# Kernel tuning notes

Measured on AMD Instinct MI355X. Metric: run time of the kernel, lower is better.

## Reference

```python
import jax, jax.numpy as jnp
import numpy as np

N_NODES = 150000   # n_users + n_entities
N_EDGES = 4800000  # nnz of sparse A_in (avg degree 32)
EMBED_DIM = 64
CONV_DIMS = [64, 32, 16]  # [embed_dim] + conv_dim_list
EPS = 1e-12  # F.normalize eps


def setup_inputs() -> dict:
    key = jax.random.key(0)
    ks = jax.random.split(key, 12)
    inp = {
        "E": jax.random.normal(ks[0], (N_NODES, EMBED_DIM), jnp.float32) * 0.1,
        "edge_vals": jax.random.uniform(ks[1], (N_EDGES,), jnp.float32),
        "rows": jax.random.randint(ks[2], (N_EDGES,), 0, N_NODES),
        "cols": jax.random.randint(ks[3], (N_EDGES,), 0, N_NODES),
    }
    i = 4
    for l in range(len(CONV_DIMS) - 1):
        din, dout = CONV_DIMS[l], CONV_DIMS[l + 1]
        scale = 1.0 / np.sqrt(din)
        inp[f"W1_{l}"] = jax.random.normal(ks[i], (dout, din), jnp.float32) * scale
        inp[f"b1_{l}"] = jax.random.normal(ks[i + 1], (dout,), jnp.float32) * 0.01
        inp[f"W2_{l}"] = jax.random.normal(ks[i + 2], (dout, din), jnp.float32) * scale
        inp[f"b2_{l}"] = jax.random.normal(ks[i + 3], (dout,), jnp.float32) * 0.01
        i += 4
    return inp


def _cf_embeddings(E, edge_vals, rows, cols, layer_params):
    """UIR_KG.calc_cf_embeddings: sparse A_in @ x, then KGAT bi-interaction."""
    N = E.shape[0]
    x = E
    outs = [x]
    for (W1, b1, W2, b2) in layer_params:
        # side = A_in @ x  as gather -> weight -> scatter-add over COO edges
        msgs = edge_vals[:, None] * x[cols]              # [n_edges, d]
        side = jax.ops.segment_sum(msgs, rows, num_segments=N)  # [N, d]
        sum_emb = jax.nn.leaky_relu((x + side) @ W1.T + b1)     # Linear1 + LeakyReLU
        bi_emb = jax.nn.leaky_relu((x * side) @ W2.T + b2)      # Linear2 + LeakyReLU
        x = sum_emb + bi_emb
        norm = jnp.linalg.norm(x, axis=1, keepdims=True)        # F.normalize(p=2, dim=1)
        outs.append(x / jnp.maximum(norm, EPS))
    return jnp.concatenate(outs, axis=1)  # [N, 64+32+16]


def reference(E, edge_vals, W1_0, b1_0, W2_0, b2_0, W1_1, b1_1, W2_1, b2_1, rows, cols):
    params = [(W1_0, b1_0, W2_0, b2_0), (W1_1, b1_1, W2_1, b2_1)]
    return _cf_embeddings(E, edge_vals, rows, cols, params)
```

## Files before the change

### kernel.cpp

```cpp
#include <hip/hip_runtime.h>


constexpr int PSHIFT = 9;
constexpr int PROWS  = 1 << PSHIFT;
constexpr int PBINS  = 512;
constexpr int GF_T   = 1024;
constexpr int GF_E   = 4096;
constexpr int GF_K   = GF_E / GF_T;

static __device__ __forceinline__ float leaky(float v) {
    return v > 0.0f ? v : 0.01f * v;
}

static __device__ __forceinline__ unsigned short f2bf_rne(float f) {
    unsigned u = __float_as_uint(f);
    return (unsigned short)((u + 0x7FFF + ((u >> 16) & 1)) >> 16);
}

static __device__ __forceinline__ float bf2f(unsigned short s) {
    return __uint_as_float(((unsigned)s) << 16);
}

__global__ void copy_E_kernel(const float* __restrict__ E, float* __restrict__ out,
                              unsigned short* __restrict__ Ebf, int N) {
    int tid = blockIdx.x * blockDim.x + threadIdx.x;
    if (tid >= N * 16) return;
    int i = tid >> 4, g = tid & 15;
    float4 v = reinterpret_cast<const float4*>(E)[(size_t)i * 16 + g];
    *reinterpret_cast<float4*>(out + (size_t)i * 112 + g * 4) = v;
    if (Ebf) {
        ushort4 b;
        b.x = f2bf_rne(v.x); b.y = f2bf_rne(v.y);
        b.z = f2bf_rne(v.z); b.w = f2bf_rne(v.w);
        *reinterpret_cast<ushort4*>(Ebf + (size_t)i * 64 + g * 4) = b;
    }
}

__global__ void part_hist_kernel(const int* __restrict__ rows, int* __restrict__ pcnt,
                                 int NE, int P) {
    extern __shared__ int h[];
    for (int i = threadIdx.x; i < P; i += blockDim.x) h[i] = 0;
    __syncthreads();
    for (int e = blockIdx.x * blockDim.x + threadIdx.x; e < NE; e += gridDim.x * blockDim.x)
        atomicAdd(&h[rows[e] >> PSHIFT], 1);
    __syncthreads();
    for (int i = threadIdx.x; i < P; i += blockDim.x) {
        int c = h[i];
        if (c) atomicAdd(&pcnt[i], c);
    }
}

__global__ __launch_bounds__(PBINS) void part_scan_kernel(
    const int* __restrict__ pcnt, int* __restrict__ pbase,
    int* __restrict__ gcur, int P, int NE) {
    __shared__ int s[PBINS];
    int v = (threadIdx.x < (unsigned)P) ? pcnt[threadIdx.x] : 0;
    s[threadIdx.x] = v;
    __syncthreads();
    for (int off = 1; off < PBINS; off <<= 1) {
        int t = (threadIdx.x >= (unsigned)off) ? s[threadIdx.x - off] : 0;
        __syncthreads();
        s[threadIdx.x] += t;
        __syncthreads();
    }
    if (threadIdx.x < (unsigned)P) {
        int ex = s[threadIdx.x] - v;
        pbase[threadIdx.x] = ex;
        gcur[threadIdx.x]  = ex;
    }
    if (threadIdx.x == 0) pbase[P] = NE;
}

__global__ __launch_bounds__(GF_T) void group_flush_kernel(
    const int* __restrict__ rows, const int* __restrict__ cols,
    const float* __restrict__ ev, int* __restrict__ gcur,
    int2* __restrict__ tmp, int NE, int P) {
    __shared__ int2 staged[GF_E];
    __shared__ unsigned short sp[GF_E];
    __shared__ int hist[PBINS], runstart[PBINS], hcur[PBINS], gbase[PBINS], scanb[PBINS];

    int e0  = blockIdx.x * GF_E;
    int cnt = min(GF_E, NE - e0);

    if (threadIdx.x < PBINS) hist[threadIdx.x] = 0;
    __syncthreads();

    int pk[GF_K], ck[GF_K], rk[GF_K];
    float vk[GF_K];
#pragma unroll
    for (int k = 0; k < GF_K; k++) {
        int idx = threadIdx.x + k * GF_T;
        if (idx < cnt) {
            int r = rows[e0 + idx];
            pk[k] = r >> PSHIFT;
            rk[k] = r & (PROWS - 1);
            ck[k] = cols[e0 + idx];
            vk[k] = ev[e0 + idx];
            atomicAdd(&hist[pk[k]], 1);
        } else pk[k] = -1;
    }
    __syncthreads();
    if (threadIdx.x < PBINS) scanb[threadIdx.x] = hist[threadIdx.x];
    __syncthreads();
    for (int off = 1; off < PBINS; off <<= 1) {
        int t = 0;
        if (threadIdx.x < PBINS && threadIdx.x >= (unsigned)off) t = scanb[threadIdx.x - off];
        __syncthreads();
        if (threadIdx.x < PBINS) scanb[threadIdx.x] += t;
        __syncthreads();
    }
    if (threadIdx.x < PBINS) {
        int ex = scanb[threadIdx.x] - hist[threadIdx.x];
        runstart[threadIdx.x] = ex;
        hcur[threadIdx.x]     = ex;
    }
    __syncthreads();
#pragma unroll
    for (int k = 0; k < GF_K; k++) {
        if (pk[k] >= 0) {
            int slot = atomicAdd(&hcur[pk[k]], 1);
            staged[slot] = make_int2(ck[k] | (rk[k] << 18), __float_as_int(vk[k]));
            sp[slot] = (unsigned short)pk[k];
        }
    }
    __syncthreads();
    if (threadIdx.x < (unsigned)P) {
        int h = hist[threadIdx.x];
        if (h > 0) gbase[threadIdx.x] = atomicAdd(&gcur[threadIdx.x], h);
    }
    __syncthreads();
#pragma unroll
    for (int k = 0; k < GF_K; k++) {
        int i = threadIdx.x + k * GF_T;
        if (i < cnt) {
            int p = sp[i];
            tmp[gbase[p] + (i - runstart[p])] = staged[i];
        }
    }
}

__global__ __launch_bounds__(PROWS) void row_sort_kernel(
    const int2* __restrict__ tmp, int2* __restrict__ pairs,
    const int* __restrict__ pbase, int* __restrict__ row_end, int N) {
    __shared__ int hist[PROWS], cur[PROWS], scanb[PROWS];
    int p     = blockIdx.x;
    int start = pbase[p];
    int end   = pbase[p + 1];
    hist[threadIdx.x] = 0;
    __syncthreads();
    for (int e = start + threadIdx.x; e < end; e += PROWS)
        atomicAdd(&hist[tmp[e].x >> 18], 1);
    __syncthreads();
    scanb[threadIdx.x] = hist[threadIdx.x];
    __syncthreads();
    for (int off = 1; off < PROWS; off <<= 1) {
        int t = (threadIdx.x >= (unsigned)off) ? scanb[threadIdx.x - off] : 0;
        __syncthreads();
        scanb[threadIdx.x] += t;
        __syncthreads();
    }
    int inc = scanb[threadIdx.x];
    cur[threadIdx.x] = start + inc - hist[threadIdx.x];
    int row = (p << PSHIFT) + threadIdx.x;
    if (row < N) row_end[row] = start + inc;
    __syncthreads();
    for (int e = start + threadIdx.x; e < end; e += PROWS) {
        int2 t = tmp[e];
        int pos = atomicAdd(&cur[t.x >> 18], 1);
        pairs[pos] = make_int2(t.x & 0x3FFFF, t.y);
    }
}

template<int DIN, int DOUT>
__global__ __launch_bounds__(256) void pull_layer_bf16_kernel(
    const float* __restrict__ x, const unsigned short* __restrict__ xb,
    const int2* __restrict__ pairs, const int* __restrict__ row_end,
    const float* __restrict__ W1, const float* __restrict__ b1,
    const float* __restrict__ W2, const float* __restrict__ b2,
    float* __restrict__ xnext, unsigned short* __restrict__ xnextb,
    float* __restrict__ out, int out_col0, int N) {
    constexpr int Q   = DIN / 4;
    constexpr int RPB = 256 / Q;
    constexpr int LD  = DIN + 4;
    constexpr int LD4 = LD / 4;
    static_assert(DOUT == 2 * Q, "thread owns exactly 2 output dims");

    __shared__ float sW1[DOUT * LD];
    __shared__ float sW2[DOUT * LD];
    __shared__ float hb[2][RPB][LD];

    for (int idx = threadIdx.x; idx < DOUT * DIN; idx += 256) {
        int j = idx / DIN, k = idx % DIN;
        sW1[j * LD + k] = W1[idx];
        sW2[j * LD + k] = W2[idx];
    }

    int lr  = threadIdx.x / Q;
    int q   = threadIdx.x % Q;
    int row = blockIdx.x * RPB + lr;

    if (row < N) {
        int start = row ? row_end[row - 1] : 0;
        int end   = row_end[row];
        const ushort4* xbv = reinterpret_cast<const ushort4*>(xb);
        float4 acc = make_float4(0.f, 0.f, 0.f, 0.f);
        int e = start;
        for (; e + 7 < end; e += 8) {
            int2 p[8]; ushort4 g[8];
#pragma unroll
            for (int k = 0; k < 8; k++) p[k] = pairs[e + k];
#pragma unroll
            for (int k = 0; k < 8; k++) g[k] = xbv[(size_t)p[k].x * Q + q];
#pragma unroll
            for (int k = 0; k < 8; k++) {
                float v = __int_as_float(p[k].y);
                acc.x += v * bf2f(g[k].x); acc.y += v * bf2f(g[k].y);
                acc.z += v * bf2f(g[k].z); acc.w += v * bf2f(g[k].w);
            }
        }
        for (; e < end; e++) {
            int2 p0 = pairs[e];
            ushort4 g0 = xbv[(size_t)p0.x * Q + q];
            float v0 = __int_as_float(p0.y);
            acc.x += v0 * bf2f(g0.x); acc.y += v0 * bf2f(g0.y);
            acc.z += v0 * bf2f(g0.z); acc.w += v0 * bf2f(g0.w);
        }
        const float4* xv = reinterpret_cast<const float4*>(x);
        float4 xr = xv[(size_t)row * Q + q];
        float4 h1 = make_float4(xr.x + acc.x, xr.y + acc.y, xr.z + acc.z, xr.w + acc.w);
        float4 h2 = make_float4(xr.x * acc.x, xr.y * acc.y, xr.z * acc.z, xr.w * acc.w);
        *reinterpret_cast<float4*>(&hb[0][lr][q * 4]) = h1;
        *reinterpret_cast<float4*>(&hb[1][lr][q * 4]) = h2;
    }
    __syncthreads();
    if (row >= N) return;

    float a0 = b1[q], a1 = b1[q + Q], a2 = b2[q], a3 = b2[q + Q];
    const float4* w1v = reinterpret_cast<const float4*>(sW1);
    const float4* w2v = reinterpret_cast<const float4*>(sW2);
    const float4* h1v = reinterpret_cast<const float4*>(&hb[0][lr][0]);
    const float4* h2v = reinterpret_cast<const float4*>(&hb[1][lr][0]);
#pragma unroll
    for (int k4 = 0; k4 < DIN / 4; k4++) {
        float4 h1 = h1v[k4];
        float4 h2 = h2v[k4];
        float4 wa = w1v[q * LD4 + k4];
        float4 wb = w1v[(q + Q) * LD4 + k4];
        float4 wc = w2v[q * LD4 + k4];
        float4 wd = w2v[(q + Q) * LD4 + k4];
        a0 += h1.x * wa.x + h1.y * wa.y + h1.z * wa.z + h1.w * wa.w;
        a1 += h1.x * wb.x + h1.y * wb.y + h1.z * wb.z + h1.w * wb.w;
        a2 += h2.x * wc.x + h2.y * wc.y + h2.z * wc.z + h2.w * wc.w;
        a3 += h2.x * wd.x + h2.y * wd.y + h2.z * wd.z + h2.w * wd.w;
    }
    float y0 = leaky(a0) + leaky(a2);
    float y1 = leaky(a1) + leaky(a3);
    float nrm = y0 * y0 + y1 * y1;
#pragma unroll
    for (int m = 1; m < Q; m <<= 1) nrm += __shfl_xor(nrm, m, 64);
    float inv = 1.0f / fmaxf(sqrtf(nrm), 1e-12f);
    if (xnext) {
        xnext[(size_t)row * DOUT + q]     = y0;
        xnext[(size_t)row * DOUT + q + Q] = y1;
    }
    if (xnextb) {
        xnextb[(size_t)row * DOUT + q]     = f2bf_rne(y0);
        xnextb[(size_t)row * DOUT + q + Q] = f2bf_rne(y1);
    }
    float* o = out + (size_t)row * 112 + out_col0;
    o[q]     = y0 * inv;
    o[q + Q] = y1 * inv;
}

template<int DIN, int DOUT>
__global__ __launch_bounds__(256) void pull_layer_kernel(
    const float* __restrict__ x, const int2* __restrict__ pairs,
    const int* __restrict__ row_end,
    const float* __restrict__ W1, const float* __restrict__ b1,
    const float* __restrict__ W2, const float* __restrict__ b2,
    float* __restrict__ xnext, float* __restrict__ out, int out_col0, int N) {
    constexpr int Q   = DIN / 4;
    constexpr int RPB = 256 / Q;
    constexpr int LD  = DIN + 4;
    constexpr int LD4 = LD / 4;
    static_assert(DOUT == 2 * Q, "thread owns exactly 2 output dims");

    __shared__ float sW1[DOUT * LD];
    __shared__ float sW2[DOUT * LD];
    __shared__ float hb[2][RPB][LD];

    for (int idx = threadIdx.x; idx < DOUT * DIN; idx += 256) {
        int j = idx / DIN, k = idx % DIN;
        sW1[j * LD + k] = W1[idx];
        sW2[j * LD + k] = W2[idx];
    }

    int lr  = threadIdx.x / Q;
    int q   = threadIdx.x % Q;
    int row = blockIdx.x * RPB + lr;

    if (row < N) {
        int start = row ? row_end[row - 1] : 0;
        int end   = row_end[row];
        const float4* xv = reinterpret_cast<const float4*>(x);
        float4 acc = make_float4(0.f, 0.f, 0.f, 0.f);
        int e = start;
        for (; e + 3 < end; e += 4) {
            int2 p0 = pairs[e];
            int2 p1 = pairs[e + 1];
            int2 p2 = pairs[e + 2];
            int2 p3 = pairs[e + 3];
            float4 g0 = xv[(size_t)p0.x * Q + q];
            float4 g1 = xv[(size_t)p1.x * Q + q];
            float4 g2 = xv[(size_t)p2.x * Q + q];
            float4 g3 = xv[(size_t)p3.x * Q + q];
            float v0 = __int_as_float(p0.y), v1 = __int_as_float(p1.y);
            float v2 = __int_as_float(p2.y), v3 = __int_as_float(p3.y);
            acc.x += v0 * g0.x; acc.y += v0 * g0.y; acc.z += v0 * g0.z; acc.w += v0 * g0.w;
            acc.x += v1 * g1.x; acc.y += v1 * g1.y; acc.z += v1 * g1.z; acc.w += v1 * g1.w;
            acc.x += v2 * g2.x; acc.y += v2 * g2.y; acc.z += v2 * g2.z; acc.w += v2 * g2.w;
            acc.x += v3 * g3.x; acc.y += v3 * g3.y; acc.z += v3 * g3.z; acc.w += v3 * g3.w;
        }
        for (; e < end; e++) {
            int2 p0 = pairs[e];
            float4 g0 = xv[(size_t)p0.x * Q + q];
            float v0 = __int_as_float(p0.y);
            acc.x += v0 * g0.x; acc.y += v0 * g0.y; acc.z += v0 * g0.z; acc.w += v0 * g0.w;
        }
        float4 xr = xv[(size_t)row * Q + q];
        float4 h1 = make_float4(xr.x + acc.x, xr.y + acc.y, xr.z + acc.z, xr.w + acc.w);
        float4 h2 = make_float4(xr.x * acc.x, xr.y * acc.y, xr.z * acc.z, xr.w * acc.w);
        *reinterpret_cast<float4*>(&hb[0][lr][q * 4]) = h1;
        *reinterpret_cast<float4*>(&hb[1][lr][q * 4]) = h2;
    }
    __syncthreads();
    if (row >= N) return;

    float a0 = b1[q], a1 = b1[q + Q], a2 = b2[q], a3 = b2[q + Q];
    const float4* w1v = reinterpret_cast<const float4*>(sW1);
    const float4* w2v = reinterpret_cast<const float4*>(sW2);
    const float4* h1v = reinterpret_cast<const float4*>(&hb[0][lr][0]);
    const float4* h2v = reinterpret_cast<const float4*>(&hb[1][lr][0]);
#pragma unroll
    for (int k4 = 0; k4 < DIN / 4; k4++) {
        float4 h1 = h1v[k4];
        float4 h2 = h2v[k4];
        float4 wa = w1v[q * LD4 + k4];
        float4 wb = w1v[(q + Q) * LD4 + k4];
        float4 wc = w2v[q * LD4 + k4];
        float4 wd = w2v[(q + Q) * LD4 + k4];
        a0 += h1.x * wa.x + h1.y * wa.y + h1.z * wa.z + h1.w * wa.w;
        a1 += h1.x * wb.x + h1.y * wb.y + h1.z * wb.z + h1.w * wb.w;
        a2 += h2.x * wc.x + h2.y * wc.y + h2.z * wc.z + h2.w * wc.w;
        a3 += h2.x * wd.x + h2.y * wd.y + h2.z * wd.z + h2.w * wd.w;
    }
    float y0 = leaky(a0) + leaky(a2);
    float y1 = leaky(a1) + leaky(a3);
    float nrm = y0 * y0 + y1 * y1;
#pragma unroll
    for (int m = 1; m < Q; m <<= 1) nrm += __shfl_xor(nrm, m, 64);
    float inv = 1.0f / fmaxf(sqrtf(nrm), 1e-12f);
    if (xnext) {
        xnext[(size_t)row * DOUT + q]     = y0;
        xnext[(size_t)row * DOUT + q + Q] = y1;
    }
    float* o = out + (size_t)row * 112 + out_col0;
    o[q]     = y0 * inv;
    o[q + Q] = y1 * inv;
}

extern "C" void kernel_launch(void* const* d_in, const int* in_sizes, int n_in,
                              void* d_out, int out_size, void* d_ws, size_t ws_size,
                              hipStream_t stream) {
    const float* Eemb = (const float*)d_in[0];
    const float* ev   = (const float*)d_in[1];
    const int*   rows = (const int*)d_in[2];
    const int*   cols = (const int*)d_in[3];
    const float* W1_0 = (const float*)d_in[4];
    const float* b1_0 = (const float*)d_in[5];
    const float* W2_0 = (const float*)d_in[6];
    const float* b2_0 = (const float*)d_in[7];
    const float* W1_1 = (const float*)d_in[8];
    const float* b1_1 = (const float*)d_in[9];
    const float* W2_1 = (const float*)d_in[10];
    const float* b2_1 = (const float*)d_in[11];
    float* out = (float*)d_out;

    int N  = in_sizes[0] / 64;
    int NE = in_sizes[1];
    int P  = (N + PROWS - 1) >> PSHIFT;

    size_t pairs_b  = (size_t)NE * sizeof(int2);
    size_t rowend_b = ((size_t)N * sizeof(int) + 255) & ~(size_t)255;
    size_t small_b  = (PBINS + (PBINS + 1) + PBINS) * sizeof(int) + 256;
    small_b = (small_b + 255) & ~(size_t)255;
    size_t x1_b     = ((size_t)N * 32 * sizeof(float) + 255) & ~(size_t)255;
    size_t ebf_b    = ((size_t)N * 64 * sizeof(unsigned short) + 255) & ~(size_t)255;
    size_t x1b_b    = (size_t)N * 32 * sizeof(unsigned short);

    char* base = (char*)d_ws;
    int2*  pairs   = (int2*)base;
    int*   row_end = (int*)(base + pairs_b);
    int*   pcnt    = (int*)(base + pairs_b + rowend_b);
    int*   pbase   = pcnt + PBINS;
    int*   gcur    = pbase + PBINS + 1;
    float* x1      = (float*)(base + pairs_b + rowend_b + small_b);
    unsigned short* Ebf = (unsigned short*)(base + pairs_b + rowend_b + small_b + x1_b);
    unsigned short* x1b = (unsigned short*)(base + pairs_b + rowend_b + small_b + x1_b + ebf_b);

    bool use_bf  = ws_size >= pairs_b + rowend_b + small_b + x1_b + ebf_b;
    bool use_bf1 = use_bf && ws_size >= pairs_b + rowend_b + small_b + x1_b + ebf_b + x1b_b;

    int2* tmp = (int2*)d_out;

    hipMemsetAsync(pcnt, 0, PBINS * sizeof(int), stream);
    part_hist_kernel<<<256, 1024, P * sizeof(int), stream>>>(rows, pcnt, NE, P);
    part_scan_kernel<<<1, PBINS, 0, stream>>>(pcnt, pbase, gcur, P, NE);
    group_flush_kernel<<<(NE + GF_E - 1) / GF_E, GF_T, 0, stream>>>(
        rows, cols, ev, gcur, tmp, NE, P);
    row_sort_kernel<<<P, PROWS, 0, stream>>>(tmp, pairs, pbase, row_end, N);

    copy_E_kernel<<<(N * 16 + 255) / 256, 256, 0, stream>>>(
        Eemb, out, use_bf ? Ebf : nullptr, N);

    if (use_bf) {
        pull_layer_bf16_kernel<64, 32><<<(N + 15) / 16, 256, 0, stream>>>(
            Eemb, Ebf, pairs, row_end, W1_0, b1_0, W2_0, b2_0,
            x1, use_bf1 ? x1b : nullptr, out, 64, N);
    } else {
        pull_layer_kernel<64, 32><<<(N + 15) / 16, 256, 0, stream>>>(
            Eemb, pairs, row_end, W1_0, b1_0, W2_0, b2_0, x1, out, 64, N);
    }
    if (use_bf1) {
        pull_layer_bf16_kernel<32, 16><<<(N + 31) / 32, 256, 0, stream>>>(
            x1, x1b, pairs, row_end, W1_1, b1_1, W2_1, b2_1,
            nullptr, nullptr, out, 96, N);
    } else {
        pull_layer_kernel<32, 16><<<(N + 31) / 32, 256, 0, stream>>>(
            x1, pairs, row_end, W1_1, b1_1, W2_1, b2_1, nullptr, out, 96, N);
    }
}
```

Measured before the change: 350.6 us.

## Widen bf16 gathers to 8 elements per thread and drop fp32 self-row reads

The pull-layer kernel now has each thread gather 8 bf16 features per edge with a 16-byte load instead of 4 with an 8-byte load. This halves the threads per row, doubles the rows per block, and issues fewer, wider gather transactions. The self row is read from the bf16 copy instead of the fp32 embedding, and the intermediate sums are staged in shared memory as bf16. Each thread now computes 4 contiguous outputs, so the output and next-layer writes are vectorized. The layer-1 fp32 buffer is no longer written, which cuts memory traffic, but bf16 rounding of x and of the hidden sums adds error.

After: 356.8 us. Within noise of the previous version (+1.8%).

```diff
diff --git a/kernel.cpp b/kernel.cpp
--- a/kernel.cpp
+++ b/kernel.cpp
@@ -17,8 +17,13 @@
     return (unsigned short)((u + 0x7FFF + ((u >> 16) & 1)) >> 16);
 }
 
-static __device__ __forceinline__ float bf2f(unsigned short s) {
-    return __uint_as_float(((unsigned)s) << 16);
+static __device__ __forceinline__ void unpack2(unsigned u, float& lo, float& hi) {
+    lo = __uint_as_float(u << 16);
+    hi = __uint_as_float(u & 0xFFFF0000u);
+}
+
+static __device__ __forceinline__ unsigned pack2(float lo, float hi) {
+    return ((unsigned)f2bf_rne(hi) << 16) | (unsigned)f2bf_rne(lo);
 }
 
 __global__ void copy_E_kernel(const float* __restrict__ E, float* __restrict__ out,
@@ -172,27 +177,28 @@
 }
 
 template<int DIN, int DOUT>
-__global__ __launch_bounds__(256) void pull_layer_bf16_kernel(
-    const float* __restrict__ x, const unsigned short* __restrict__ xb,
+__global__ __launch_bounds__(256) void pull_layer_b2_kernel(
+    const unsigned short* __restrict__ xb,
     const int2* __restrict__ pairs, const int* __restrict__ row_end,
     const float* __restrict__ W1, const float* __restrict__ b1,
     const float* __restrict__ W2, const float* __restrict__ b2,
-    float* __restrict__ xnext, unsigned short* __restrict__ xnextb,
+    unsigned short* __restrict__ xnextb,
     float* __restrict__ out, int out_col0, int N) {
-    constexpr int Q   = DIN / 4;
+    constexpr int Q   = DIN / 8;
     constexpr int RPB = 256 / Q;
-    constexpr int LD  = DIN + 4;
-    constexpr int LD4 = LD / 4;
-    static_assert(DOUT == 2 * Q, "thread owns exactly 2 output dims");
-
-    __shared__ float sW1[DOUT * LD];
-    __shared__ float sW2[DOUT * LD];
-    __shared__ float hb[2][RPB][LD];
+    constexpr int JT  = DOUT / Q;
+    constexpr int LDU = DIN + 8;
+    constexpr int LDW = DIN + 4;
+    static_assert(JT == 4, "thread owns 4 contiguous outputs");
+
+    __shared__ float sW1[DOUT * LDW];
+    __shared__ float sW2[DOUT * LDW];
+    __shared__ unsigned short hb[2][RPB][LDU];
 
     for (int idx = threadIdx.x; idx < DOUT * DIN; idx += 256) {
         int j = idx / DIN, k = idx % DIN;
-        sW1[j * LD + k] = W1[idx];
-        sW2[j * LD + k] = W2[idx];
+        sW1[j * LDW + k] = W1[idx];
+        sW2[j * LDW + k] = W2[idx];
     }
 
     int lr  = threadIdx.x / Q;
@@ -202,11 +208,11 @@
     if (row < N) {
         int start = row ? row_end[row - 1] : 0;
         int end   = row_end[row];
-        const ushort4* xbv = reinterpret_cast<const ushort4*>(xb);
-        float4 acc = make_float4(0.f, 0.f, 0.f, 0.f);
+        const uint4* xbv = reinterpret_cast<const uint4*>(xb);
+        float acc[8] = {0.f, 0.f, 0.f, 0.f, 0.f, 0.f, 0.f, 0.f};
         int e = start;
         for (; e + 7 < end; e += 8) {
-            int2 p[8]; ushort4 g[8];
+            int2 p[8]; uint4 g[8];
 #pragma unroll
             for (int k = 0; k < 8; k++) p[k] = pairs[e + k];
 #pragma unroll
@@ -214,62 +220,86 @@
 #pragma unroll
             for (int k = 0; k < 8; k++) {
                 float v = __int_as_float(p[k].y);
-                acc.x += v * bf2f(g[k].x); acc.y += v * bf2f(g[k].y);
-                acc.z += v * bf2f(g[k].z); acc.w += v * bf2f(g[k].w);
+                float lo, hi;
+                unpack2(g[k].x, lo, hi); acc[0] += v * lo; acc[1] += v * hi;
+                unpack2(g[k].y, lo, hi); acc[2] += v * lo; acc[3] += v * hi;
+                unpack2(g[k].z, lo, hi); acc[4] += v * lo; acc[5] += v * hi;
+                unpack2(g[k].w, lo, hi); acc[6] += v * lo; acc[7] += v * hi;
             }
         }
         for (; e < end; e++) {
             int2 p0 = pairs[e];
-            ushort4 g0 = xbv[(size_t)p0.x * Q + q];
+            uint4 g0 = xbv[(size_t)p0.x * Q + q];
             float v0 = __int_as_float(p0.y);
-            acc.x += v0 * bf2f(g0.x); acc.y += v0 * bf2f(g0.y);
-            acc.z += v0 * bf2f(g0.z); acc.w += v0 * bf2f(g0.w);
-        }
-        const float4* xv = reinterpret_cast<const float4*>(x);
-        float4 xr = xv[(size_t)row * Q + q];
-        float4 h1 = make_float4(xr.x + acc.x, xr.y + acc.y, xr.z + acc.z, xr.w + acc.w);
-        float4 h2 = make_float4(xr.x * acc.x, xr.y * acc.y, xr.z * acc.z, xr.w * acc.w);
-        *reinterpret_cast<float4*>(&hb[0][lr][q * 4]) = h1;
-        *reinterpret_cast<float4*>(&hb[1][lr][q * 4]) = h2;
+            float lo, hi;
+            unpack2(g0.x, lo, hi); acc[0] += v0 * lo; acc[1] += v0 * hi;
+            unpack2(g0.y, lo, hi); acc[2] += v0 * lo; acc[3] += v0 * hi;
+            unpack2(g0.z, lo, hi); acc[4] += v0 * lo; acc[5] += v0 * hi;
+            unpack2(g0.w, lo, hi); acc[6] += v0 * lo; acc[7] += v0 * hi;
+        }
+        uint4 xr = xbv[(size_t)row * Q + q];
+        float xf[8];
+        unpack2(xr.x, xf[0], xf[1]);
+        unpack2(xr.y, xf[2], xf[3]);
+        unpack2(xr.z, xf[4], xf[5]);
+        unpack2(xr.w, xf[6], xf[7]);
+        uint4 s1, s2;
+        s1.x = pack2(xf[0] + acc[0], xf[1] + acc[1]);
+        s1.y = pack2(xf[2] + acc[2], xf[3] + acc[3]);
+        s1.z = pack2(xf[4] + acc[4], xf[5] + acc[5]);
+        s1.w = pack2(xf[6] + acc[6], xf[7] + acc[7]);
+        s2.x = pack2(xf[0] * acc[0], xf[1] * acc[1]);
+        s2.y = pack2(xf[2] * acc[2], xf[3] * acc[3]);
+        s2.z = pack2(xf[4] * acc[4], xf[5] * acc[5]);
+        s2.w = pack2(xf[6] * acc[6], xf[7] * acc[7]);
+        *reinterpret_cast<uint4*>(&hb[0][lr][q * 8]) = s1;
+        *reinterpret_cast<uint4*>(&hb[1][lr][q * 8]) = s2;
     }
     __syncthreads();
     if (row >= N) return;
 
-    float a0 = b1[q], a1 = b1[q + Q], a2 = b2[q], a3 = b2[q + Q];
-    const float4* w1v = reinterpret_cast<const float4*>(sW1);
-    const float4* w2v = reinterpret_cast<const float4*>(sW2);
-    const float4* h1v = reinterpret_cast<const float4*>(&hb[0][lr][0]);
-    const float4* h2v = reinterpret_cast<const float4*>(&hb[1][lr][0]);
-#pragma unroll
-    for (int k4 = 0; k4 < DIN / 4; k4++) {
-        float4 h1 = h1v[k4];
-        float4 h2 = h2v[k4];
-        float4 wa = w1v[q * LD4 + k4];
-        float4 wb = w1v[(q + Q) * LD4 + k4];
-        float4 wc = w2v[q * LD4 + k4];
-        float4 wd = w2v[(q + Q) * LD4 + k4];
-        a0 += h1.x * wa.x + h1.y * wa.y + h1.z * wa.z + h1.w * wa.w;
-        a1 += h1.x * wb.x + h1.y * wb.y + h1.z * wb.z + h1.w * wb.w;
-        a2 += h2.x * wc.x + h2.y * wc.y + h2.z * wc.z + h2.w * wc.w;
-        a3 += h2.x * wd.x + h2.y * wd.y + h2.z * wd.z + h2.w * wd.w;
-    }
-    float y0 = leaky(a0) + leaky(a2);
-    float y1 = leaky(a1) + leaky(a3);
-    float nrm = y0 * y0 + y1 * y1;
+    int j0 = q * JT;
+    float a1[4] = {b1[j0], b1[j0 + 1], b1[j0 + 2], b1[j0 + 3]};
+    float a2[4] = {b2[j0], b2[j0 + 1], b2[j0 + 2], b2[j0 + 3]};
+    const uint4* h1r = reinterpret_cast<const uint4*>(&hb[0][lr][0]);
+    const uint4* h2r = reinterpret_cast<const uint4*>(&hb[1][lr][0]);
+#pragma unroll
+    for (int c = 0; c < DIN / 8; c++) {
+        uint4 u1 = h1r[c], u2 = h2r[c];
+        float f1[8], f2[8];
+        unpack2(u1.x, f1[0], f1[1]); unpack2(u1.y, f1[2], f1[3]);
+        unpack2(u1.z, f1[4], f1[5]); unpack2(u1.w, f1[6], f1[7]);
+        unpack2(u2.x, f2[0], f2[1]); unpack2(u2.y, f2[2], f2[3]);
+        unpack2(u2.z, f2[4], f2[5]); unpack2(u2.w, f2[6], f2[7]);
+#pragma unroll
+        for (int jj = 0; jj < 4; jj++) {
+            const float4* w1p = reinterpret_cast<const float4*>(&sW1[(j0 + jj) * LDW + c * 8]);
+            const float4* w2p = reinterpret_cast<const float4*>(&sW2[(j0 + jj) * LDW + c * 8]);
+            float4 wa = w1p[0], wb = w1p[1];
+            float4 wc = w2p[0], wd = w2p[1];
+            a1[jj] += f1[0] * wa.x + f1[1] * wa.y + f1[2] * wa.z + f1[3] * wa.w
+                    + f1[4] * wb.x + f1[5] * wb.y + f1[6] * wb.z + f1[7] * wb.w;
+            a2[jj] += f2[0] * wc.x + f2[1] * wc.y + f2[2] * wc.z + f2[3] * wc.w
+                    + f2[4] * wd.x + f2[5] * wd.y + f2[6] * wd.z + f2[7] * wd.w;
+        }
+    }
+    float y[4], nrm = 0.f;
+#pragma unroll
+    for (int jj = 0; jj < 4; jj++) {
+        y[jj] = leaky(a1[jj]) + leaky(a2[jj]);
+        nrm += y[jj] * y[jj];
+    }
 #pragma unroll
     for (int m = 1; m < Q; m <<= 1) nrm += __shfl_xor(nrm, m, 64);
     float inv = 1.0f / fmaxf(sqrtf(nrm), 1e-12f);
-    if (xnext) {
-        xnext[(size_t)row * DOUT + q]     = y0;
-        xnext[(size_t)row * DOUT + q + Q] = y1;
-    }
     if (xnextb) {
-        xnextb[(size_t)row * DOUT + q]     = f2bf_rne(y0);
-        xnextb[(size_t)row * DOUT + q + Q] = f2bf_rne(y1);
-    }
-    float* o = out + (size_t)row * 112 + out_col0;
-    o[q]     = y0 * inv;
-    o[q + Q] = y1 * inv;
+        ushort4 xo;
+        xo.x = f2bf_rne(y[0]); xo.y = f2bf_rne(y[1]);
+        xo.z = f2bf_rne(y[2]); xo.w = f2bf_rne(y[3]);
+        *reinterpret_cast<ushort4*>(xnextb + (size_t)row * DOUT + j0) = xo;
+    }
+    float4 ov = make_float4(y[0] * inv, y[1] * inv, y[2] * inv, y[3] * inv);
+    *reinterpret_cast<float4*>(out + (size_t)row * 112 + out_col0 + j0) = ov;
 }
 
 template<int DIN, int DOUT>
@@ -394,9 +424,9 @@
     size_t rowend_b = ((size_t)N * sizeof(int) + 255) & ~(size_t)255;
     size_t small_b  = (PBINS + (PBINS + 1) + PBINS) * sizeof(int) + 256;
     small_b = (small_b + 255) & ~(size_t)255;
-    size_t x1_b     = ((size_t)N * 32 * sizeof(float) + 255) & ~(size_t)255;
     size_t ebf_b    = ((size_t)N * 64 * sizeof(unsigned short) + 255) & ~(size_t)255;
     size_t x1b_b    = (size_t)N * 32 * sizeof(unsigned short);
+    size_t x1_b     = (size_t)N * 32 * sizeof(float);
 
     char* base = (char*)d_ws;
     int2*  pairs   = (int2*)base;
@@ -404,12 +434,11 @@
     int*   pcnt    = (int*)(base + pairs_b + rowend_b);
     int*   pbase   = pcnt + PBINS;
     int*   gcur    = pbase + PBINS + 1;
-    float* x1      = (float*)(base + pairs_b + rowend_b + small_b);
-    unsigned short* Ebf = (unsigned short*)(base + pairs_b + rowend_b + small_b + x1_b);
-    unsigned short* x1b = (unsigned short*)(base + pairs_b + rowend_b + small_b + x1_b + ebf_b);
-
-    bool use_bf  = ws_size >= pairs_b + rowend_b + small_b + x1_b + ebf_b;
-    bool use_bf1 = use_bf && ws_size >= pairs_b + rowend_b + small_b + x1_b + ebf_b + x1b_b;
+    unsigned short* Ebf = (unsigned short*)(base + pairs_b + rowend_b + small_b);
+    unsigned short* x1b = (unsigned short*)(base + pairs_b + rowend_b + small_b + ebf_b);
+    float* x1 = (float*)(base + pairs_b + rowend_b + small_b);
+
+    bool use_bf = ws_size >= pairs_b + rowend_b + small_b + ebf_b + x1b_b;
 
     int2* tmp = (int2*)d_out;
 
@@ -424,18 +453,13 @@
         Eemb, out, use_bf ? Ebf : nullptr, N);
 
     if (use_bf) {
-        pull_layer_bf16_kernel<64, 32><<<(N + 15) / 16, 256, 0, stream>>>(
-            Eemb, Ebf, pairs, row_end, W1_0, b1_0, W2_0, b2_0,
-            x1, use_bf1 ? x1b : nullptr, out, 64, N);
+        pull_layer_b2_kernel<64, 32><<<(N + 31) / 32, 256, 0, stream>>>(
+            Ebf, pairs, row_end, W1_0, b1_0, W2_0, b2_0, x1b, out, 64, N);
+        pull_layer_b2_kernel<32, 16><<<(N + 63) / 64, 256, 0, stream>>>(
+            x1b, pairs, row_end, W1_1, b1_1, W2_1, b2_1, nullptr, out, 96, N);
     } else {
         pull_layer_kernel<64, 32><<<(N + 15) / 16, 256, 0, stream>>>(
             Eemb, pairs, row_end, W1_0, b1_0, W2_0, b2_0, x1, out, 64, N);
-    }
-    if (use_bf1) {
-        pull_layer_bf16_kernel<32, 16><<<(N + 31) / 32, 256, 0, stream>>>(
-            x1, x1b, pairs, row_end, W1_1, b1_1, W2_1, b2_1,
-            nullptr, nullptr, out, 96, N);
-    } else {
         pull_layer_kernel<32, 16><<<(N + 31) / 32, 256, 0, stream>>>(
             x1, pairs, row_end, W1_1, b1_1, W2_1, b2_1, nullptr, out, 96, N);
     }
```
